# Kernel tuning notes

Hardware: AMD Instinct MI355X
Metric: run time of the kernel (lower is better)

Reference implementation:

```python
import jax, jax.numpy as jnp
import numpy as np

N_NODES = 50000
N_EDGES = 1600000
IN_DIM = 128
HIDDEN = 256
N_CLASSES = 2
N_GRAPHS = 512
BN_EPS = 1e-5


def setup_inputs() -> dict:
    key = jax.random.key(0)
    ks = jax.random.split(key, 12)
    x = jax.random.normal(ks[0], (N_NODES, IN_DIM), dtype=jnp.float32)
    edge_index = jax.random.randint(ks[1], (2, N_EDGES), 0, N_NODES, dtype=jnp.int64)
    batch = jnp.sort(jax.random.randint(ks[2], (N_NODES,), 0, N_GRAPHS, dtype=jnp.int64))
    s1 = 1.0 / np.sqrt(IN_DIM)
    s2 = 1.0 / np.sqrt(HIDDEN)
    return {
        "x": x,
        "edge_index": edge_index,
        "batch": batch,
        # GIN MLP: Linear(in,hidden) -> BN -> ReLU -> Linear(hidden,hidden)
        "W1": jax.random.uniform(ks[3], (IN_DIM, HIDDEN), jnp.float32, -s1, s1),
        "b1": jnp.zeros((HIDDEN,), jnp.float32),
        "g1": jnp.ones((HIDDEN,), jnp.float32),
        "be1": jnp.zeros((HIDDEN,), jnp.float32),
        "W2": jax.random.uniform(ks[4], (HIDDEN, HIDDEN), jnp.float32, -s2, s2),
        "b2": jnp.zeros((HIDDEN,), jnp.float32),
        # attention gate: Linear(hidden, 1)
        "Wg": jax.random.uniform(ks[5], (HIDDEN, 1), jnp.float32, -s2, s2),
        "bg": jnp.zeros((1,), jnp.float32),
        # head: BN(hidden) -> Dropout(eval: identity) -> Linear(hidden, n_classes)
        "g2": jnp.ones((HIDDEN,), jnp.float32),
        "be2": jnp.zeros((HIDDEN,), jnp.float32),
        "Wh": jax.random.uniform(ks[6], (HIDDEN, N_CLASSES), jnp.float32, -s2, s2),
        "bh": jnp.zeros((N_CLASSES,), jnp.float32),
    }


def _batchnorm(h, gamma, beta):
    # training-mode BN: batch statistics over axis 0 (biased variance, as torch)
    mu = jnp.mean(h, axis=0)
    var = jnp.mean(jnp.square(h - mu), axis=0)
    return gamma * (h - mu) * jax.lax.rsqrt(var + BN_EPS) + beta


def reference(x, edge_index, batch, W1, b1, g1, be1, W2, b2, Wg, bg, g2, be2, Wh, bh):
    src, dst = edge_index[0], edge_index[1]
    # GINConv (eps=0): agg_i = sum_{j->i} x_j ; h = MLP(x + agg)
    agg = jax.ops.segment_sum(x[src], dst, num_segments=N_NODES)  # [N, in_dim]
    h = x + agg
    h = h @ W1 + b1                      # [N, hidden]
    h = jax.nn.relu(_batchnorm(h, g1, be1))
    h = h @ W2 + b2                      # [N, hidden]
    h = jax.nn.relu(h)                   # outer F.relu in forward
    # AttentionalAggregation: segment softmax of gate, weighted sum per graph
    gate = h @ Wg + bg                   # [N, 1]
    m = jax.ops.segment_max(gate, batch, num_segments=N_GRAPHS)  # [G, 1]
    e = jnp.exp(gate - m[batch])
    s = jax.ops.segment_sum(e, batch, num_segments=N_GRAPHS)     # [G, 1]
    alpha = e / s[batch]                 # [N, 1]
    pooled = jax.ops.segment_sum(alpha * h, batch, num_segments=N_GRAPHS)  # [G, hidden]
    # head: BN -> (Dropout eval = identity) -> Linear -> log_softmax
    z = _batchnorm(pooled, g2, be2) @ Wh + bh  # [G, n_classes]
    return jax.nn.log_softmax(z, axis=-1)
```

## Files before the change

### kernel.cpp

```cpp
#include <hip/hip_runtime.h>

typedef unsigned int u32;
typedef unsigned short ushort_t;
typedef __attribute__((ext_vector_type(8))) short bf16x8;
typedef __attribute__((ext_vector_type(4))) float f32x4;

__device__ __forceinline__ float bf2f_lo(u32 u){
  union{u32 i; float f;} v; v.i = u<<16; return v.f;
}
__device__ __forceinline__ float bf2f_hi(u32 u){
  union{u32 i; float f;} v; v.i = u & 0xFFFF0000u; return v.f;
}
__device__ __forceinline__ float bf2f_s(ushort_t u){
  union{u32 i; float f;} v; v.i = ((u32)u)<<16; return v.f;
}
__device__ __forceinline__ u32 pack2bf(float a, float b){
  union{float f; u32 i;} va, vb; va.f=a; vb.f=b;
  u32 ra = (va.i + 0x7FFF + ((va.i>>16)&1)) >> 16;
  u32 rb = (vb.i + 0x7FFF + ((vb.i>>16)&1)) & 0xFFFF0000u;
  return ra | rb;
}
__device__ __forceinline__ ushort_t f2bf1(float f){
  union{float f; u32 i;} v; v.f=f;
  u32 r = v.i + 0x7FFF + ((v.i>>16)&1);
  return (ushort_t)(r>>16);
}

__global__ __launch_bounds__(256) void to_bf16(const float* __restrict__ x, u32* __restrict__ xb, long n4){
  long i = (long)blockIdx.x*256 + threadIdx.x;
  if(i*4 >= n4*4) return;
  float4 v = ((const float4*)x)[i];
  uint2 o; o.x = pack2bf(v.x, v.y); o.y = pack2bf(v.z, v.w);
  ((uint2*)xb)[i] = o;
}

__global__ __launch_bounds__(256) void transpose_w(const float* __restrict__ W, ushort_t* __restrict__ Wt, int K){
  int n = blockIdx.x;
  for(int k = threadIdx.x; k < K; k += 256){
    Wt[(size_t)n*K + k] = f2bf1(W[(size_t)k*256 + n]);
  }
}

__global__ __launch_bounds__(256) void hist_k(const int* __restrict__ dst, int* __restrict__ bcount,
                                              int E, int N, int NB){
  __shared__ int h[1024];
  for(int i=threadIdx.x; i<1024; i+=256) h[i]=0;
  __syncthreads();
  int e0 = blockIdx.x*8192;
  int e1 = min(e0+8192, E);
  for(int i=e0+threadIdx.x; i<e1; i+=256){
    int d = dst[i];
    if((u32)d >= (u32)N) d = 0;
    atomicAdd(&h[d>>6], 1);
  }
  __syncthreads();
  for(int i=threadIdx.x; i<NB; i+=256){
    int v = h[i];
    if(v) atomicAdd(&bcount[i], v);
  }
}

__global__ __launch_bounds__(256) void bucket_scan(const int* __restrict__ bcount, int* __restrict__ bstart,
                                                   int* __restrict__ bcursor, int NB){
  __shared__ int tsum[256];
  int t = threadIdx.x;
  int base = t*4;
  int a0 = (base+0<NB)?bcount[base+0]:0;
  int a1 = (base+1<NB)?bcount[base+1]:0;
  int a2 = (base+2<NB)?bcount[base+2]:0;
  int a3 = (base+3<NB)?bcount[base+3]:0;
  int s0=a0, s1=s0+a1, s2=s1+a2, s3=s2+a3;
  tsum[t]=s3; __syncthreads();
  #pragma unroll
  for(int d=1; d<256; d<<=1){
    int v = (t>=d)?tsum[t-d]:0;
    __syncthreads();
    tsum[t]+=v;
    __syncthreads();
  }
  int prev = (t>0)?tsum[t-1]:0;
  if(base+0<NB){ bstart[base+0]=prev;    bcursor[(base+0)*16]=0; }
  if(base+1<NB){ bstart[base+1]=prev+s0; bcursor[(base+1)*16]=0; }
  if(base+2<NB){ bstart[base+2]=prev+s1; bcursor[(base+2)*16]=0; }
  if(base+3<NB){ bstart[base+3]=prev+s2; bcursor[(base+3)*16]=0; }
  if(t==255){ bstart[NB]=prev+s3; }
}

__global__ __launch_bounds__(256) void binscatter2(const int* __restrict__ src, const int* __restrict__ dst,
                                                   const int* __restrict__ bstart, int* __restrict__ bcursor,
                                                   u32* __restrict__ pairs, int E, int N, int NB){
  __shared__ int hist[1024];
  __shared__ int base[1024];
  int e0 = blockIdx.x*8192;
  int e1 = min(e0+8192, E);
  for(int i=threadIdx.x; i<NB; i+=256) hist[i]=0;
  __syncthreads();
  for(int i=e0+threadIdx.x; i<e1; i+=256){
    int d = dst[i];
    if((u32)d >= (u32)N) d = 0;
    atomicAdd(&hist[d>>6], 1);
  }
  __syncthreads();
  for(int i=threadIdx.x; i<NB; i+=256){
    int c = hist[i];
    base[i] = c ? (bstart[i] + atomicAdd(&bcursor[i*16], c)) : 0;
    hist[i] = 0;
  }
  __syncthreads();
  for(int i=e0+threadIdx.x; i<e1; i+=256){
    int d = dst[i]; if((u32)d >= (u32)N) d = 0;
    int s = src[i]; if((u32)s >= (u32)N) s = 0;
    int b = d>>6;
    int loc = atomicAdd(&hist[b], 1);
    pairs[base[b]+loc] = (u32)s | (((u32)(d & 63))<<17);
  }
}

#define BCAP2 2560
__global__ __launch_bounds__(512) void gather_bucket(const u32* __restrict__ xb,
                                                     const u32* __restrict__ pairs,
                                                     const int* __restrict__ bstart,
                                                     u32* __restrict__ h0b, int N){
  __shared__ int lsrc[BCAP2];
  __shared__ int dcnt[32];
  __shared__ int dstart[33];
  __shared__ int dcur[32];
  __shared__ int s_fits;
  int b    = blockIdx.x >> 1;
  int half = blockIdx.x & 1;
  int p0 = bstart[b], p1 = bstart[b+1];
  int cnt = p1 - p0;
  int tid = threadIdx.x;
  if(tid < 32) dcnt[tid] = 0;
  __syncthreads();
  for(int i=tid; i<cnt; i+=512){
    u32 u = pairs[p0+i];
    int loc = (u>>17)&63;
    if((loc>>5) == half) atomicAdd(&dcnt[loc&31], 1);
  }
  __syncthreads();
  if(tid==0){
    int run=0;
    #pragma unroll
    for(int j=0;j<32;j++){ dstart[j]=run; dcur[j]=run; run+=dcnt[j]; }
    dstart[32]=run;
    s_fits = (run <= BCAP2) ? 1 : 0;
  }
  __syncthreads();
  bool fits = (s_fits != 0);
  if(fits){
    for(int i=tid; i<cnt; i+=512){
      u32 u = pairs[p0+i];
      int loc = (u>>17)&63;
      if((loc>>5) == half){
        int pos = atomicAdd(&dcur[loc&31], 1);
        lsrc[pos] = (int)(u & 0x1FFFFu);
      }
    }
    __syncthreads();
  }
  const uint4* xr = (const uint4*)xb;
  int slot = tid >> 4;
  int c = tid & 15;
  int node = b*64 + half*32 + slot;
  if(node >= N) return;
  uint4 xv = xr[(size_t)node*16 + c];
  float acc[8] = {
    bf2f_lo(xv.x), bf2f_hi(xv.x), bf2f_lo(xv.y), bf2f_hi(xv.y),
    bf2f_lo(xv.z), bf2f_hi(xv.z), bf2f_lo(xv.w), bf2f_hi(xv.w) };
  if(fits){
    int ds = dstart[slot], de = dstart[slot+1];
    int j = ds;
    for(; j+8 <= de; j += 8){
      int s0=lsrc[j+0], s1=lsrc[j+1], s2=lsrc[j+2], s3=lsrc[j+3];
      int s4=lsrc[j+4], s5=lsrc[j+5], s6=lsrc[j+6], s7=lsrc[j+7];
      uint4 v0 = xr[(size_t)s0*16 + c];
      uint4 v1 = xr[(size_t)s1*16 + c];
      uint4 v2 = xr[(size_t)s2*16 + c];
      uint4 v3 = xr[(size_t)s3*16 + c];
      uint4 v4 = xr[(size_t)s4*16 + c];
      uint4 v5 = xr[(size_t)s5*16 + c];
      uint4 v6 = xr[(size_t)s6*16 + c];
      uint4 v7 = xr[(size_t)s7*16 + c];
      acc[0]+=bf2f_lo(v0.x)+bf2f_lo(v1.x)+bf2f_lo(v2.x)+bf2f_lo(v3.x)
             +bf2f_lo(v4.x)+bf2f_lo(v5.x)+bf2f_lo(v6.x)+bf2f_lo(v7.x);
      acc[1]+=bf2f_hi(v0.x)+bf2f_hi(v1.x)+bf2f_hi(v2.x)+bf2f_hi(v3.x)
             +bf2f_hi(v4.x)+bf2f_hi(v5.x)+bf2f_hi(v6.x)+bf2f_hi(v7.x);
      acc[2]+=bf2f_lo(v0.y)+bf2f_lo(v1.y)+bf2f_lo(v2.y)+bf2f_lo(v3.y)
             +bf2f_lo(v4.y)+bf2f_lo(v5.y)+bf2f_lo(v6.y)+bf2f_lo(v7.y);
      acc[3]+=bf2f_hi(v0.y)+bf2f_hi(v1.y)+bf2f_hi(v2.y)+bf2f_hi(v3.y)
             +bf2f_hi(v4.y)+bf2f_hi(v5.y)+bf2f_hi(v6.y)+bf2f_hi(v7.y);
      acc[4]+=bf2f_lo(v0.z)+bf2f_lo(v1.z)+bf2f_lo(v2.z)+bf2f_lo(v3.z)
             +bf2f_lo(v4.z)+bf2f_lo(v5.z)+bf2f_lo(v6.z)+bf2f_lo(v7.z);
      acc[5]+=bf2f_hi(v0.z)+bf2f_hi(v1.z)+bf2f_hi(v2.z)+bf2f_hi(v3.z)
             +bf2f_hi(v4.z)+bf2f_hi(v5.z)+bf2f_hi(v6.z)+bf2f_hi(v7.z);
      acc[6]+=bf2f_lo(v0.w)+bf2f_lo(v1.w)+bf2f_lo(v2.w)+bf2f_lo(v3.w)
             +bf2f_lo(v4.w)+bf2f_lo(v5.w)+bf2f_lo(v6.w)+bf2f_lo(v7.w);
      acc[7]+=bf2f_hi(v0.w)+bf2f_hi(v1.w)+bf2f_hi(v2.w)+bf2f_hi(v3.w)
             +bf2f_hi(v4.w)+bf2f_hi(v5.w)+bf2f_hi(v6.w)+bf2f_hi(v7.w);
    }
    for(; j < de; j++){
      int s = lsrc[j];
      uint4 v = xr[(size_t)s*16 + c];
      acc[0]+=bf2f_lo(v.x); acc[1]+=bf2f_hi(v.x);
      acc[2]+=bf2f_lo(v.y); acc[3]+=bf2f_hi(v.y);
      acc[4]+=bf2f_lo(v.z); acc[5]+=bf2f_hi(v.z);
      acc[6]+=bf2f_lo(v.w); acc[7]+=bf2f_hi(v.w);
    }
  } else {
    int want = half*32 + slot;
    for(int i=0;i<cnt;i++){
      u32 u = pairs[p0+i];
      if((int)((u>>17)&63) == want){
        int s = (int)(u & 0x1FFFFu);
        uint4 v = xr[(size_t)s*16 + c];
        acc[0]+=bf2f_lo(v.x); acc[1]+=bf2f_hi(v.x);
        acc[2]+=bf2f_lo(v.y); acc[3]+=bf2f_hi(v.y);
        acc[4]+=bf2f_lo(v.z); acc[5]+=bf2f_hi(v.z);
        acc[6]+=bf2f_lo(v.w); acc[7]+=bf2f_hi(v.w);
      }
    }
  }
  uint4 o;
  o.x = pack2bf(acc[0],acc[1]); o.y = pack2bf(acc[2],acc[3]);
  o.z = pack2bf(acc[4],acc[5]); o.w = pack2bf(acc[6],acc[7]);
  ((uint4*)h0b)[(size_t)node*16 + c] = o;
}

template<int K, bool BNA, bool RELUOUT, bool GATE, bool ABF16, bool OUTBF16, bool STATS>
__global__ __launch_bounds__(512) void gemm_mfma(const void* __restrict__ Ap, const ushort_t* __restrict__ Wt,
                                                 const float* __restrict__ bias,
                                                 const float* __restrict__ scale, const float* __restrict__ shift,
                                                 void* __restrict__ Cp, int M,
                                                 const float* __restrict__ Wg, const float* __restrict__ bg,
                                                 float* __restrict__ gate,
                                                 float* __restrict__ psum, float* __restrict__ pq, int NS){
  __shared__ uint4 Al[8*129];
  __shared__ uint4 Bl[8*257];
  __shared__ float gacc[128];
  __shared__ float sstat[512];
  const int tid  = threadIdx.x;
  const int lane = tid & 63;
  const int wave = tid >> 6;
  const int lm   = lane & 15;
  const int q    = lane >> 4;
  const int mhalf= wave >> 2;
  const int nq   = wave & 3;
  const int m0   = blockIdx.x * 128;

  if(GATE && tid < 128) gacc[tid] = 0.f;
  if(STATS){ sstat[tid] = 0.f; }

  f32x4 acc[4][4];
  #pragma unroll
  for(int i=0;i<4;i++)
    #pragma unroll
    for(int j=0;j<4;j++) acc[i][j] = (f32x4){0.f,0.f,0.f,0.f};

  for(int k0=0; k0<K; k0+=64){
    #pragma unroll
    for(int i=0;i<2;i++){
      int idx = tid*2 + i;
      int m = idx >> 3, c = idx & 7;
      int grow = m0 + m;
      int kk = k0 + c*8;
      uint4 v = make_uint4(0,0,0,0);
      if(ABF16){
        if(grow < M) v = *(const uint4*)((const ushort_t*)Ap + (size_t)grow*K + kk);
        if(BNA){
          float f0=bf2f_lo(v.x), f1=bf2f_hi(v.x), f2=bf2f_lo(v.y), f3=bf2f_hi(v.y);
          float f4=bf2f_lo(v.z), f5=bf2f_hi(v.z), f6=bf2f_lo(v.w), f7=bf2f_hi(v.w);
          float4 s0 = *(const float4*)(scale+kk),  s1 = *(const float4*)(scale+kk+4);
          float4 t0 = *(const float4*)(shift+kk),  t1 = *(const float4*)(shift+kk+4);
          f0=fmaxf(fmaf(s0.x,f0,t0.x),0.f); f1=fmaxf(fmaf(s0.y,f1,t0.y),0.f);
          f2=fmaxf(fmaf(s0.z,f2,t0.z),0.f); f3=fmaxf(fmaf(s0.w,f3,t0.w),0.f);
          f4=fmaxf(fmaf(s1.x,f4,t1.x),0.f); f5=fmaxf(fmaf(s1.y,f5,t1.y),0.f);
          f6=fmaxf(fmaf(s1.z,f6,t1.z),0.f); f7=fmaxf(fmaf(s1.w,f7,t1.w),0.f);
          v.x = pack2bf(f0,f1); v.y = pack2bf(f2,f3);
          v.z = pack2bf(f4,f5); v.w = pack2bf(f6,f7);
        }
      } else {
        float4 u0 = make_float4(0,0,0,0), u1 = make_float4(0,0,0,0);
        if(grow < M){
          u0 = *(const float4*)((const float*)Ap + (size_t)grow*K + kk);
          u1 = *(const float4*)((const float*)Ap + (size_t)grow*K + kk + 4);
        }
        if(BNA){
          float4 s0 = *(const float4*)(scale+kk),  s1 = *(const float4*)(scale+kk+4);
          float4 t0 = *(const float4*)(shift+kk),  t1 = *(const float4*)(shift+kk+4);
          u0.x=fmaxf(fmaf(s0.x,u0.x,t0.x),0.f); u0.y=fmaxf(fmaf(s0.y,u0.y,t0.y),0.f);
          u0.z=fmaxf(fmaf(s0.z,u0.z,t0.z),0.f); u0.w=fmaxf(fmaf(s0.w,u0.w,t0.w),0.f);
          u1.x=fmaxf(fmaf(s1.x,u1.x,t1.x),0.f); u1.y=fmaxf(fmaf(s1.y,u1.y,t1.y),0.f);
          u1.z=fmaxf(fmaf(s1.z,u1.z,t1.z),0.f); u1.w=fmaxf(fmaf(s1.w,u1.w,t1.w),0.f);
        }
        v.x = pack2bf(u0.x,u0.y); v.y = pack2bf(u0.z,u0.w);
        v.z = pack2bf(u1.x,u1.y); v.w = pack2bf(u1.z,u1.w);
      }
      Al[c*129 + m] = v;
    }
    #pragma unroll
    for(int i=0;i<4;i++){
      int idx = tid*4 + i;
      int n = idx >> 3, c = idx & 7;
      Bl[c*257 + n] = *(const uint4*)(Wt + (size_t)n*K + k0 + c*8);
    }
    __syncthreads();
    #pragma unroll
    for(int ks=0; ks<2; ks++){
      int cc = ks*4 + q;
      bf16x8 af[4], bfr[4];
      #pragma unroll
      for(int mi=0; mi<4; mi++)
        af[mi] = *((const bf16x8*)&Al[cc*129 + mhalf*64 + mi*16 + lm]);
      #pragma unroll
      for(int ni=0; ni<4; ni++)
        bfr[ni] = *((const bf16x8*)&Bl[cc*257 + nq*64 + ni*16 + lm]);
      #pragma unroll
      for(int mi=0; mi<4; mi++)
        #pragma unroll
        for(int ni=0; ni<4; ni++)
          acc[mi][ni] = __builtin_amdgcn_mfma_f32_16x16x32_bf16(af[mi], bfr[ni], acc[mi][ni], 0, 0, 0);
    }
    __syncthreads();
  }

  float bb[4], wgv[4];
  float cs[4] = {0.f,0.f,0.f,0.f};
  float cq[4] = {0.f,0.f,0.f,0.f};
  #pragma unroll
  for(int ni=0; ni<4; ni++){
    int col = nq*64 + ni*16 + lm;
    bb[ni] = bias[col];
    if(GATE) wgv[ni] = Wg[col];
  }
  #pragma unroll
  for(int mi=0; mi<4; mi++){
    int rowloc0 = mhalf*64 + mi*16 + q*4;
    float gp[4] = {0.f,0.f,0.f,0.f};
    #pragma unroll
    for(int ni=0; ni<4; ni++){
      int col = nq*64 + ni*16 + lm;
      f32x4 o = acc[mi][ni];
      #pragma unroll
      for(int r=0; r<4; r++){
        float v = o[r] + bb[ni];
        if(RELUOUT) v = fmaxf(v, 0.f);
        int row = m0 + rowloc0 + r;
        if(row < M){
          if(OUTBF16) ((ushort_t*)Cp)[(size_t)row*256 + col] = f2bf1(v);
          else        ((float*)Cp)[(size_t)row*256 + col] = v;
          if(STATS){ cs[ni] += v; cq[ni] = fmaf(v, v, cq[ni]); }
        }
        if(GATE) gp[r] = fmaf(v, wgv[ni], gp[r]);
      }
    }
    if(GATE){
      #pragma unroll
      for(int r=0; r<4; r++){
        if(m0 + rowloc0 + r < M) atomicAdd(&gacc[rowloc0 + r], gp[r]);
      }
    }
  }
  if(STATS){
    __syncthreads();
    #pragma unroll
    for(int ni=0; ni<4; ni++){
      int col = nq*64 + ni*16 + lm;
      atomicAdd(&sstat[col], cs[ni]);
      atomicAdd(&sstat[256+col], cq[ni]);
    }
    __syncthreads();
    if(tid < 256){
      psum[(size_t)tid*NS + blockIdx.x] = sstat[tid];
      pq[(size_t)tid*NS + blockIdx.x]   = sstat[256+tid];
    }
  }
  if(GATE){
    __syncthreads();
    if(tid < 128){
      int row = m0 + tid;
      if(row < M) gate[row] = gacc[tid] + bg[0];
    }
  }
}

__global__ __launch_bounds__(256) void col_stats2(const float* __restrict__ h, float* __restrict__ psum,
                                                  float* __restrict__ pq, int M, int rpb, int nblk){
  int b = blockIdx.x;
  int g = threadIdx.x >> 6;
  int lane = threadIdx.x & 63;
  int c0 = lane*4;
  int r0 = b*rpb;
  int r1 = min(r0+rpb, M);
  float4 s4 = make_float4(0.f,0.f,0.f,0.f);
  float4 q4 = make_float4(0.f,0.f,0.f,0.f);
  for(int r=r0+g; r<r1; r+=4){
    float4 v = *(const float4*)(h + (size_t)r*256 + c0);
    s4.x+=v.x; s4.y+=v.y; s4.z+=v.z; s4.w+=v.w;
    q4.x=fmaf(v.x,v.x,q4.x); q4.y=fmaf(v.y,v.y,q4.y);
    q4.z=fmaf(v.z,v.z,q4.z); q4.w=fmaf(v.w,v.w,q4.w);
  }
  __shared__ float ls[1024];
  __shared__ float lq[1024];
  *(float4*)&ls[g*256+c0] = s4;
  *(float4*)&lq[g*256+c0] = q4;
  __syncthreads();
  if(threadIdx.x < 64){
    #pragma unroll
    for(int j=0;j<4;j++){
      int c = c0+j;
      float s = ls[c]+ls[256+c]+ls[512+c]+ls[768+c];
      float q = lq[c]+lq[256+c]+lq[512+c]+lq[768+c];
      psum[(size_t)c*nblk + b] = s;
      pq[(size_t)c*nblk + b]   = q;
    }
  }
}

__global__ __launch_bounds__(512) void stats_fin(const float* __restrict__ psum, const float* __restrict__ pq,
                                                 const float* __restrict__ gamma, const float* __restrict__ beta,
                                                 float* __restrict__ scale, float* __restrict__ shift,
                                                 int nblk, float invM){
  __shared__ float red[512];
  int t = threadIdx.x;
  const float* src = (t<256) ? (psum + (size_t)t*nblk) : (pq + (size_t)(t-256)*nblk);
  float s = 0.f;
  for(int i=0;i<nblk;i+=4){
    float4 v = *(const float4*)(src+i);
    s += v.x+v.y+v.z+v.w;
  }
  red[t]=s; __syncthreads();
  if(t<256){
    float mu  = red[t]*invM;
    float var = fmaxf(red[256+t]*invM - mu*mu, 0.f);
    float sc  = gamma[t] * rsqrtf(var + 1e-5f);
    scale[t]=sc; shift[t]=fmaf(-mu, sc, beta[t]);
  }
}

__global__ __launch_bounds__(512) void pool_k(const ushort_t* __restrict__ h2b, const float* __restrict__ gate,
                                              const int* __restrict__ batch, float* __restrict__ pooled, int N){
  int g = blockIdx.x;
  __shared__ int sb[2];
  __shared__ float red[8];
  __shared__ float s_m, s_inv;
  __shared__ float la[256];
  __shared__ float sa0[512];
  __shared__ float sa1[512];
  int t = threadIdx.x;
  if(t < 2){
    int target = g + t;
    int lo=0, hi=N;
    while(lo<hi){ int mid=(lo+hi)>>1; if(batch[mid] < target) lo=mid+1; else hi=mid; }
    sb[t] = lo;
  }
  __syncthreads();
  int beg = sb[0], end = sb[1];
  float mx = -1e30f;
  for(int i=beg+t; i<end; i+=512) mx = fmaxf(mx, gate[i]);
  #pragma unroll
  for(int d=32; d>0; d>>=1) mx = fmaxf(mx, __shfl_down(mx, d, 64));
  if((t&63)==0) red[t>>6] = mx;
  __syncthreads();
  if(t==0){
    float m = red[0];
    #pragma unroll
    for(int w=1; w<8; w++) m = fmaxf(m, red[w]);
    s_m = m;
  }
  __syncthreads();
  float m = s_m;
  float s = 0.f;
  for(int i=beg+t; i<end; i+=512) s += expf(gate[i]-m);
  #pragma unroll
  for(int d=32; d>0; d>>=1) s += __shfl_down(s, d, 64);
  if((t&63)==0) red[t>>6] = s;
  __syncthreads();
  if(t==0){
    float tot = 0.f;
    #pragma unroll
    for(int w=0; w<8; w++) tot += red[w];
    s_inv = (tot > 0.f) ? 1.f/tot : 0.f;
  }
  __syncthreads();
  float inv = s_inv;
  const u32* h2w = (const u32*)h2b;
  int colpair = t & 127;
  int rowgrp  = t >> 7;
  float a0 = 0.f, a1 = 0.f;
  for(int ci=beg; ci<end; ci+=256){
    int chunk = min(256, end-ci);
    if(t < 256) la[t] = (t < chunk) ? expf(gate[ci+t]-m)*inv : 0.f;
    __syncthreads();
    for(int j=rowgrp; j<chunk; j+=4){
      u32 h = h2w[(size_t)(ci+j)*128 + colpair];
      float w = la[j];
      a0 = fmaf(w, bf2f_lo(h), a0);
      a1 = fmaf(w, bf2f_hi(h), a1);
    }
    __syncthreads();
  }
  sa0[t] = a0; sa1[t] = a1;
  __syncthreads();
  if(t < 128){
    float r0 = sa0[t] + sa0[128+t] + sa0[256+t] + sa0[384+t];
    float r1 = sa1[t] + sa1[128+t] + sa1[256+t] + sa1[384+t];
    pooled[g*256 + t*2]   = r0;
    pooled[g*256 + t*2+1] = r1;
  }
}

__global__ __launch_bounds__(256) void head_k(const float* __restrict__ pooled,
                                              const float* __restrict__ sc2, const float* __restrict__ sh2,
                                              const float* __restrict__ Wh, const float* __restrict__ bh,
                                              float* __restrict__ out, int G){
  int w = (blockIdx.x*256 + threadIdx.x) >> 6;
  int l = threadIdx.x & 63;
  if(w >= G) return;
  float4 v  = *(const float4*)(pooled + (size_t)w*256 + l*4);
  float4 sc = *(const float4*)(sc2 + l*4);
  float4 sh = *(const float4*)(sh2 + l*4);
  float vv[4] = { fmaf(sc.x,v.x,sh.x), fmaf(sc.y,v.y,sh.y), fmaf(sc.z,v.z,sh.z), fmaf(sc.w,v.w,sh.w) };
  float4 w0 = *(const float4*)(Wh + (size_t)l*8);
  float4 w1 = *(const float4*)(Wh + (size_t)l*8 + 4);
  float a0 = vv[0]*w0.x + vv[1]*w0.z + vv[2]*w1.x + vv[3]*w1.z;
  float a1 = vv[0]*w0.y + vv[1]*w0.w + vv[2]*w1.y + vv[3]*w1.w;
  #pragma unroll
  for(int d=32; d>0; d>>=1){ a0 += __shfl_down(a0,d,64); a1 += __shfl_down(a1,d,64); }
  if(l==0){
    float z0 = a0 + bh[0];
    float z1 = a1 + bh[1];
    float mz = fmaxf(z0,z1);
    float lse = mz + logf(expf(z0-mz) + expf(z1-mz));
    out[w*2]   = z0 - lse;
    out[w*2+1] = z1 - lse;
  }
}

extern "C" void kernel_launch(void* const* d_in, const int* in_sizes, int n_in,
                              void* d_out, int out_size, void* d_ws, size_t ws_size,
                              hipStream_t stream){
  const float* x   = (const float*)d_in[0];
  const int*   ei  = (const int*)d_in[1];
  const int*   bat = (const int*)d_in[2];
  const float* W1  = (const float*)d_in[3];
  const float* b1  = (const float*)d_in[4];
  const float* g1  = (const float*)d_in[5];
  const float* be1 = (const float*)d_in[6];
  const float* W2  = (const float*)d_in[7];
  const float* b2  = (const float*)d_in[8];
  const float* Wg  = (const float*)d_in[9];
  const float* bg  = (const float*)d_in[10];
  const float* g2  = (const float*)d_in[11];
  const float* be2 = (const float*)d_in[12];
  const float* Wh  = (const float*)d_in[13];
  const float* bh  = (const float*)d_in[14];

  const int N = in_sizes[0] / 128;
  const int E = in_sizes[1] / 2;
  const int G = out_size / 2;
  const int NB = (N + 63) >> 6;
  const int NS1 = 512;
  const int NBLK2 = 64;

  char* ws = (char*)d_ws;
  u32*   h0b    = (u32*)ws;
  u32*   xb     = (u32*)(ws + 12800000);
  u32*   pairs  = (u32*)(ws + 25600000);
  int*   bcount = (int*)(ws + 32000000);
  int*   bstart = (int*)(ws + 32004352);
  int*   bcursor= (int*)(ws + 32008704);
  ushort_t* h2b = (ushort_t*)ws;
  u32*   h1b    = (u32*)(ws + 51200000);
  char*  p2 = ws + 102400000;
  float* psum1 = (float*)p2;          p2 += 256*NS1*4;
  float* pq1   = (float*)p2;          p2 += 256*NS1*4;
  float* psum2 = (float*)p2;          p2 += 256*NBLK2*4;
  float* pq2   = (float*)p2;          p2 += 256*NBLK2*4;
  float* sc1   = (float*)p2;          p2 += 1024;
  float* sh1   = (float*)p2;          p2 += 1024;
  float* gate  = (float*)p2;          p2 += (size_t)N*4 + 4096;
  float* pooled= (float*)p2;          p2 += (size_t)G*256*4;
  float* sc2   = (float*)p2;          p2 += 1024;
  float* sh2   = (float*)p2;          p2 += 1024;
  ushort_t* W1t = (ushort_t*)p2;      p2 += 256*128*2;
  ushort_t* W2t = (ushort_t*)p2;      p2 += 256*256*2;

  const int* src = ei;
  const int* dst = ei + E;

  hipMemsetAsync(bcount, 0, (size_t)NB*4, stream);
  hipMemsetAsync(psum1, 0, (size_t)256*NS1*4, stream);
  hipMemsetAsync(pq1,   0, (size_t)256*NS1*4, stream);

  transpose_w<<<256, 256, 0, stream>>>(W1, W1t, 128);
  transpose_w<<<256, 256, 0, stream>>>(W2, W2t, 256);
  long n4 = (long)N*128/4;
  to_bf16    <<<(int)((n4+255)/256), 256, 0, stream>>>(x, xb, n4);

  int nchunk = (E + 8191)/8192;
  hist_k     <<<nchunk, 256, 0, stream>>>(dst, bcount, E, N, NB);
  bucket_scan<<<1, 256, 0, stream>>>(bcount, bstart, bcursor, NB);
  binscatter2<<<nchunk, 256, 0, stream>>>(src, dst, bstart, bcursor, pairs, E, N, NB);
  gather_bucket<<<NB*2, 512, 0, stream>>>(xb, pairs, bstart, h0b, N);

  int gblocks = (N + 127)/128;
  gemm_mfma<128,false,false,false,true,true,true><<<gblocks, 512, 0, stream>>>(
      h0b, W1t, b1, nullptr, nullptr, h1b, N, nullptr, nullptr, nullptr, psum1, pq1, NS1);
  stats_fin  <<<1, 512, 0, stream>>>(psum1, pq1, g1, be1, sc1, sh1, NS1, 1.0f/(float)N);
  gemm_mfma<256,true,true,true,true,true,false><<<gblocks, 512, 0, stream>>>(
      h1b, W2t, b2, sc1, sh1, h2b, N, Wg, bg, gate, nullptr, nullptr, 0);

  pool_k <<<G, 512, 0, stream>>>(h2b, gate, bat, pooled, N);
  int rpb2 = (G + NBLK2 - 1)/NBLK2;
  col_stats2 <<<NBLK2, 256, 0, stream>>>(pooled, psum2, pq2, G, rpb2, NBLK2);
  stats_fin  <<<1, 512, 0, stream>>>(psum2, pq2, g2, be2, sc2, sh2, NBLK2, 1.0f/(float)G);
  head_k <<<(G+3)/4, 256, 0, stream>>>(pooled, sc2, sh2, Wh, bh, (float*)d_out, G);
}
```

Before: 353.8 us.

## Fuse prep kernels, drop bucket histogram/scan via fixed-capacity buckets, fuse head

Merges the bf16 conversion, both weight transposes and the cursor reset into one prep launch. Removes the histogram and scan passes by giving each 64-node bucket a fixed capacity, with an overflow list for edges past it. The gather now uses one block per bucket instead of two, and the head BN statistics, normalization and classifier run in a single one-block kernel. This cuts launches, memsets and a pass over dst, at the cost of a serial scan of the overflow list per node if any bucket overflows, and a single-block head.

```diff
diff --git a/kernel.cpp b/kernel.cpp
--- a/kernel.cpp
+++ b/kernel.cpp
@@ -4,6 +4,9 @@
 typedef unsigned short ushort_t;
 typedef __attribute__((ext_vector_type(8))) short bf16x8;
 typedef __attribute__((ext_vector_type(4))) float f32x4;
+
+#define PCAP 3072
+#define OVFCAP 1600000
 
 __device__ __forceinline__ float bf2f_lo(u32 u){
   union{u32 i; float f;} v; v.i = u<<16; return v.f;
@@ -26,69 +29,33 @@
   return (ushort_t)(r>>16);
 }
 
-__global__ __launch_bounds__(256) void to_bf16(const float* __restrict__ x, u32* __restrict__ xb, long n4){
-  long i = (long)blockIdx.x*256 + threadIdx.x;
-  if(i*4 >= n4*4) return;
-  float4 v = ((const float4*)x)[i];
-  uint2 o; o.x = pack2bf(v.x, v.y); o.y = pack2bf(v.z, v.w);
-  ((uint2*)xb)[i] = o;
-}
-
-__global__ __launch_bounds__(256) void transpose_w(const float* __restrict__ W, ushort_t* __restrict__ Wt, int K){
-  int n = blockIdx.x;
-  for(int k = threadIdx.x; k < K; k += 256){
-    Wt[(size_t)n*K + k] = f2bf1(W[(size_t)k*256 + n]);
-  }
-}
-
-__global__ __launch_bounds__(256) void hist_k(const int* __restrict__ dst, int* __restrict__ bcount,
-                                              int E, int N, int NB){
-  __shared__ int h[1024];
-  for(int i=threadIdx.x; i<1024; i+=256) h[i]=0;
-  __syncthreads();
-  int e0 = blockIdx.x*8192;
-  int e1 = min(e0+8192, E);
-  for(int i=e0+threadIdx.x; i<e1; i+=256){
-    int d = dst[i];
-    if((u32)d >= (u32)N) d = 0;
-    atomicAdd(&h[d>>6], 1);
-  }
-  __syncthreads();
-  for(int i=threadIdx.x; i<NB; i+=256){
-    int v = h[i];
-    if(v) atomicAdd(&bcount[i], v);
-  }
-}
-
-__global__ __launch_bounds__(256) void bucket_scan(const int* __restrict__ bcount, int* __restrict__ bstart,
-                                                   int* __restrict__ bcursor, int NB){
-  __shared__ int tsum[256];
-  int t = threadIdx.x;
-  int base = t*4;
-  int a0 = (base+0<NB)?bcount[base+0]:0;
-  int a1 = (base+1<NB)?bcount[base+1]:0;
-  int a2 = (base+2<NB)?bcount[base+2]:0;
-  int a3 = (base+3<NB)?bcount[base+3]:0;
-  int s0=a0, s1=s0+a1, s2=s1+a2, s3=s2+a3;
-  tsum[t]=s3; __syncthreads();
-  #pragma unroll
-  for(int d=1; d<256; d<<=1){
-    int v = (t>=d)?tsum[t-d]:0;
-    __syncthreads();
-    tsum[t]+=v;
-    __syncthreads();
-  }
-  int prev = (t>0)?tsum[t-1]:0;
-  if(base+0<NB){ bstart[base+0]=prev;    bcursor[(base+0)*16]=0; }
-  if(base+1<NB){ bstart[base+1]=prev+s0; bcursor[(base+1)*16]=0; }
-  if(base+2<NB){ bstart[base+2]=prev+s1; bcursor[(base+2)*16]=0; }
-  if(base+3<NB){ bstart[base+3]=prev+s2; bcursor[(base+3)*16]=0; }
-  if(t==255){ bstart[NB]=prev+s3; }
-}
-
-__global__ __launch_bounds__(256) void binscatter2(const int* __restrict__ src, const int* __restrict__ dst,
-                                                   const int* __restrict__ bstart, int* __restrict__ bcursor,
-                                                   u32* __restrict__ pairs, int E, int N, int NB){
+__global__ __launch_bounds__(256) void prep(const float* __restrict__ x, u32* __restrict__ xb, long nconv,
+                                            const float* __restrict__ W1, ushort_t* __restrict__ W1t,
+                                            const float* __restrict__ W2, ushort_t* __restrict__ W2t,
+                                            int* __restrict__ bcursor, int* __restrict__ ovf_cnt, int NB){
+  long blk = blockIdx.x;
+  int tid = threadIdx.x;
+  if(blk < nconv){
+    long i = blk*256 + tid;
+    float4 v = ((const float4*)x)[i];
+    uint2 o; o.x = pack2bf(v.x, v.y); o.y = pack2bf(v.z, v.w);
+    ((uint2*)xb)[i] = o;
+  } else if(blk < nconv + 256){
+    int n = (int)(blk - nconv);
+    for(int k = tid; k < 128; k += 256) W1t[(size_t)n*128 + k] = f2bf1(W1[(size_t)k*256 + n]);
+  } else if(blk < nconv + 512){
+    int n = (int)(blk - nconv - 256);
+    for(int k = tid; k < 256; k += 256) W2t[(size_t)n*256 + k] = f2bf1(W2[(size_t)k*256 + n]);
+  } else {
+    for(int i = tid; i < NB*16; i += 256) bcursor[i] = 0;
+    if(tid == 0) *ovf_cnt = 0;
+  }
+}
+
+__global__ __launch_bounds__(256) void binscatter_direct(const int* __restrict__ src, const int* __restrict__ dst,
+                                                         int* __restrict__ bcursor, u32* __restrict__ pairs,
+                                                         int* __restrict__ ovf, int* __restrict__ ovf_cnt,
+                                                         int E, int N, int NB){
   __shared__ int hist[1024];
   __shared__ int base[1024];
   int e0 = blockIdx.x*8192;
@@ -103,7 +70,7 @@
   __syncthreads();
   for(int i=threadIdx.x; i<NB; i+=256){
     int c = hist[i];
-    base[i] = c ? (bstart[i] + atomicAdd(&bcursor[i*16], c)) : 0;
+    base[i] = c ? atomicAdd(&bcursor[i*16], c) : 0;
     hist[i] = 0;
   }
   __syncthreads();
@@ -112,64 +79,66 @@
     int s = src[i]; if((u32)s >= (u32)N) s = 0;
     int b = d>>6;
     int loc = atomicAdd(&hist[b], 1);
-    pairs[base[b]+loc] = (u32)s | (((u32)(d & 63))<<17);
-  }
-}
-
-#define BCAP2 2560
+    int pos = base[b] + loc;
+    if(pos < PCAP){
+      pairs[(size_t)b*PCAP + pos] = (u32)s | (((u32)(d & 63))<<17);
+    } else {
+      int o = atomicAdd(ovf_cnt, 1);
+      if(o < OVFCAP){ ovf[2*o] = s; ovf[2*o+1] = d; }
+    }
+  }
+}
+
 __global__ __launch_bounds__(512) void gather_bucket(const u32* __restrict__ xb,
                                                      const u32* __restrict__ pairs,
-                                                     const int* __restrict__ bstart,
+                                                     const int* __restrict__ bcursor,
+                                                     const int* __restrict__ ovf, const int* __restrict__ ovf_cnt,
                                                      u32* __restrict__ h0b, int N){
-  __shared__ int lsrc[BCAP2];
-  __shared__ int dcnt[32];
-  __shared__ int dstart[33];
-  __shared__ int dcur[32];
-  __shared__ int s_fits;
-  int b    = blockIdx.x >> 1;
-  int half = blockIdx.x & 1;
-  int p0 = bstart[b], p1 = bstart[b+1];
-  int cnt = p1 - p0;
+  __shared__ int lsrc[PCAP];
+  __shared__ int dcnt[64];
+  __shared__ int dstart[65];
+  __shared__ int dcur[64];
+  __shared__ int s_ovfn;
+  int b = blockIdx.x;
   int tid = threadIdx.x;
-  if(tid < 32) dcnt[tid] = 0;
-  __syncthreads();
-  for(int i=tid; i<cnt; i+=512){
-    u32 u = pairs[p0+i];
-    int loc = (u>>17)&63;
-    if((loc>>5) == half) atomicAdd(&dcnt[loc&31], 1);
+  int cnt = bcursor[b*16];
+  if(cnt < 0) cnt = 0;
+  int cl = min(cnt, PCAP);
+  if(tid < 64) dcnt[tid] = 0;
+  if(tid == 0){ int o = *ovf_cnt; s_ovfn = (o < 0) ? 0 : min(o, OVFCAP); }
+  __syncthreads();
+  const u32* mypairs = pairs + (size_t)b*PCAP;
+  for(int i=tid; i<cl; i+=512){
+    u32 u = mypairs[i];
+    atomicAdd(&dcnt[(u>>17)&63], 1);
   }
   __syncthreads();
   if(tid==0){
     int run=0;
     #pragma unroll
-    for(int j=0;j<32;j++){ dstart[j]=run; dcur[j]=run; run+=dcnt[j]; }
-    dstart[32]=run;
-    s_fits = (run <= BCAP2) ? 1 : 0;
-  }
-  __syncthreads();
-  bool fits = (s_fits != 0);
-  if(fits){
-    for(int i=tid; i<cnt; i+=512){
-      u32 u = pairs[p0+i];
-      int loc = (u>>17)&63;
-      if((loc>>5) == half){
-        int pos = atomicAdd(&dcur[loc&31], 1);
-        lsrc[pos] = (int)(u & 0x1FFFFu);
-      }
-    }
-    __syncthreads();
-  }
+    for(int j=0;j<64;j++){ dstart[j]=run; dcur[j]=run; run+=dcnt[j]; }
+    dstart[64]=run;
+  }
+  __syncthreads();
+  for(int i=tid; i<cl; i+=512){
+    u32 u = mypairs[i];
+    int pos = atomicAdd(&dcur[(u>>17)&63], 1);
+    lsrc[pos] = (int)(u & 0x1FFFFu);
+  }
+  __syncthreads();
+  int ovfn = s_ovfn;
   const uint4* xr = (const uint4*)xb;
   int slot = tid >> 4;
   int c = tid & 15;
-  int node = b*64 + half*32 + slot;
-  if(node >= N) return;
-  uint4 xv = xr[(size_t)node*16 + c];
-  float acc[8] = {
-    bf2f_lo(xv.x), bf2f_hi(xv.x), bf2f_lo(xv.y), bf2f_hi(xv.y),
-    bf2f_lo(xv.z), bf2f_hi(xv.z), bf2f_lo(xv.w), bf2f_hi(xv.w) };
-  if(fits){
-    int ds = dstart[slot], de = dstart[slot+1];
+  for(int pass=0; pass<2; pass++){
+    int r = pass*32 + slot;
+    int node = b*64 + r;
+    if(node >= N) continue;
+    uint4 xv = xr[(size_t)node*16 + c];
+    float acc[8] = {
+      bf2f_lo(xv.x), bf2f_hi(xv.x), bf2f_lo(xv.y), bf2f_hi(xv.y),
+      bf2f_lo(xv.z), bf2f_hi(xv.z), bf2f_lo(xv.w), bf2f_hi(xv.w) };
+    int ds = dstart[r], de = dstart[r+1];
     int j = ds;
     for(; j+8 <= de; j += 8){
       int s0=lsrc[j+0], s1=lsrc[j+1], s2=lsrc[j+2], s3=lsrc[j+3];
@@ -207,24 +176,24 @@
       acc[4]+=bf2f_lo(v.z); acc[5]+=bf2f_hi(v.z);
       acc[6]+=bf2f_lo(v.w); acc[7]+=bf2f_hi(v.w);
     }
-  } else {
-    int want = half*32 + slot;
-    for(int i=0;i<cnt;i++){
-      u32 u = pairs[p0+i];
-      if((int)((u>>17)&63) == want){
-        int s = (int)(u & 0x1FFFFu);
-        uint4 v = xr[(size_t)s*16 + c];
-        acc[0]+=bf2f_lo(v.x); acc[1]+=bf2f_hi(v.x);
-        acc[2]+=bf2f_lo(v.y); acc[3]+=bf2f_hi(v.y);
-        acc[4]+=bf2f_lo(v.z); acc[5]+=bf2f_hi(v.z);
-        acc[6]+=bf2f_lo(v.w); acc[7]+=bf2f_hi(v.w);
+    if(ovfn > 0){
+      for(int i=0;i<ovfn;i++){
+        int s = ovf[2*i], d = ovf[2*i+1];
+        if(d == node){
+          if((u32)s >= (u32)N) s = 0;
+          uint4 v = xr[(size_t)s*16 + c];
+          acc[0]+=bf2f_lo(v.x); acc[1]+=bf2f_hi(v.x);
+          acc[2]+=bf2f_lo(v.y); acc[3]+=bf2f_hi(v.y);
+          acc[4]+=bf2f_lo(v.z); acc[5]+=bf2f_hi(v.z);
+          acc[6]+=bf2f_lo(v.w); acc[7]+=bf2f_hi(v.w);
+        }
       }
     }
-  }
-  uint4 o;
-  o.x = pack2bf(acc[0],acc[1]); o.y = pack2bf(acc[2],acc[3]);
-  o.z = pack2bf(acc[4],acc[5]); o.w = pack2bf(acc[6],acc[7]);
-  ((uint4*)h0b)[(size_t)node*16 + c] = o;
+    uint4 o;
+    o.x = pack2bf(acc[0],acc[1]); o.y = pack2bf(acc[2],acc[3]);
+    o.z = pack2bf(acc[4],acc[5]); o.w = pack2bf(acc[6],acc[7]);
+    ((uint4*)h0b)[(size_t)node*16 + c] = o;
+  }
 }
 
 template<int K, bool BNA, bool RELUOUT, bool GATE, bool ABF16, bool OUTBF16, bool STATS>
@@ -384,51 +353,20 @@
   }
 }
 
-__global__ __launch_bounds__(256) void col_stats2(const float* __restrict__ h, float* __restrict__ psum,
-                                                  float* __restrict__ pq, int M, int rpb, int nblk){
-  int b = blockIdx.x;
-  int g = threadIdx.x >> 6;
-  int lane = threadIdx.x & 63;
-  int c0 = lane*4;
-  int r0 = b*rpb;
-  int r1 = min(r0+rpb, M);
-  float4 s4 = make_float4(0.f,0.f,0.f,0.f);
-  float4 q4 = make_float4(0.f,0.f,0.f,0.f);
-  for(int r=r0+g; r<r1; r+=4){
-    float4 v = *(const float4*)(h + (size_t)r*256 + c0);
-    s4.x+=v.x; s4.y+=v.y; s4.z+=v.z; s4.w+=v.w;
-    q4.x=fmaf(v.x,v.x,q4.x); q4.y=fmaf(v.y,v.y,q4.y);
-    q4.z=fmaf(v.z,v.z,q4.z); q4.w=fmaf(v.w,v.w,q4.w);
-  }
-  __shared__ float ls[1024];
-  __shared__ float lq[1024];
-  *(float4*)&ls[g*256+c0] = s4;
-  *(float4*)&lq[g*256+c0] = q4;
-  __syncthreads();
-  if(threadIdx.x < 64){
-    #pragma unroll
-    for(int j=0;j<4;j++){
-      int c = c0+j;
-      float s = ls[c]+ls[256+c]+ls[512+c]+ls[768+c];
-      float q = lq[c]+lq[256+c]+lq[512+c]+lq[768+c];
-      psum[(size_t)c*nblk + b] = s;
-      pq[(size_t)c*nblk + b]   = q;
-    }
-  }
-}
-
 __global__ __launch_bounds__(512) void stats_fin(const float* __restrict__ psum, const float* __restrict__ pq,
                                                  const float* __restrict__ gamma, const float* __restrict__ beta,
                                                  float* __restrict__ scale, float* __restrict__ shift,
-                                                 int nblk, float invM){
+                                                 int nblk, int NS, float invM){
   __shared__ float red[512];
   int t = threadIdx.x;
-  const float* src = (t<256) ? (psum + (size_t)t*nblk) : (pq + (size_t)(t-256)*nblk);
+  const float* src = (t<256) ? (psum + (size_t)t*NS) : (pq + (size_t)(t-256)*NS);
   float s = 0.f;
-  for(int i=0;i<nblk;i+=4){
+  int i = 0;
+  for(; i+4 <= nblk; i += 4){
     float4 v = *(const float4*)(src+i);
     s += v.x+v.y+v.z+v.w;
   }
+  for(; i < nblk; i++) s += src[i];
   red[t]=s; __syncthreads();
   if(t<256){
     float mu  = red[t]*invM;
@@ -510,30 +448,48 @@
   }
 }
 
-__global__ __launch_bounds__(256) void head_k(const float* __restrict__ pooled,
-                                              const float* __restrict__ sc2, const float* __restrict__ sh2,
-                                              const float* __restrict__ Wh, const float* __restrict__ bh,
-                                              float* __restrict__ out, int G){
-  int w = (blockIdx.x*256 + threadIdx.x) >> 6;
-  int l = threadIdx.x & 63;
-  if(w >= G) return;
-  float4 v  = *(const float4*)(pooled + (size_t)w*256 + l*4);
-  float4 sc = *(const float4*)(sc2 + l*4);
-  float4 sh = *(const float4*)(sh2 + l*4);
-  float vv[4] = { fmaf(sc.x,v.x,sh.x), fmaf(sc.y,v.y,sh.y), fmaf(sc.z,v.z,sh.z), fmaf(sc.w,v.w,sh.w) };
-  float4 w0 = *(const float4*)(Wh + (size_t)l*8);
-  float4 w1 = *(const float4*)(Wh + (size_t)l*8 + 4);
-  float a0 = vv[0]*w0.x + vv[1]*w0.z + vv[2]*w1.x + vv[3]*w1.z;
-  float a1 = vv[0]*w0.y + vv[1]*w0.w + vv[2]*w1.y + vv[3]*w1.w;
-  #pragma unroll
-  for(int d=32; d>0; d>>=1){ a0 += __shfl_down(a0,d,64); a1 += __shfl_down(a1,d,64); }
-  if(l==0){
+__global__ __launch_bounds__(512) void head_fused(const float* __restrict__ pooled,
+                                                  const float* __restrict__ g2, const float* __restrict__ be2,
+                                                  const float* __restrict__ Wh, const float* __restrict__ bh,
+                                                  float* __restrict__ out, int G){
+  __shared__ float red[512];
+  __shared__ float sc[256], sh[256];
+  __shared__ float wh[512];
+  int t = threadIdx.x;
+  {
+    int c = t & 255;
+    bool wantq = (t >= 256);
+    float s = 0.f;
+    for(int r=0; r<G; r++){
+      float v = pooled[(size_t)r*256 + c];
+      s = wantq ? fmaf(v, v, s) : (s + v);
+    }
+    red[t] = s;
+  }
+  if(t < 512) wh[t] = Wh[t];
+  __syncthreads();
+  if(t < 256){
+    float invG = 1.f/(float)G;
+    float mu  = red[t]*invG;
+    float var = fmaxf(red[256+t]*invG - mu*mu, 0.f);
+    float s   = g2[t] * rsqrtf(var + 1e-5f);
+    sc[t] = s; sh[t] = fmaf(-mu, s, be2[t]);
+  }
+  __syncthreads();
+  if(t < G){
+    float a0 = 0.f, a1 = 0.f;
+    const float* row = pooled + (size_t)t*256;
+    for(int c=0; c<256; c++){
+      float vv = fmaf(sc[c], row[c], sh[c]);
+      a0 = fmaf(vv, wh[2*c],   a0);
+      a1 = fmaf(vv, wh[2*c+1], a1);
+    }
     float z0 = a0 + bh[0];
     float z1 = a1 + bh[1];
     float mz = fmaxf(z0,z1);
     float lse = mz + logf(expf(z0-mz) + expf(z1-mz));
-    out[w*2]   = z0 - lse;
-    out[w*2+1] = z1 - lse;
+    out[t*2]   = z0 - lse;
+    out[t*2+1] = z1 - lse;
   }
 }
 
@@ -560,60 +516,44 @@
   const int E = in_sizes[1] / 2;
   const int G = out_size / 2;
   const int NB = (N + 63) >> 6;
-  const int NS1 = 512;
-  const int NBLK2 = 64;
+  const int gblocks = (N + 127)/128;
+  const int NS1 = (gblocks + 7) & ~7;
 
   char* ws = (char*)d_ws;
   u32*   h0b    = (u32*)ws;
   u32*   xb     = (u32*)(ws + 12800000);
   u32*   pairs  = (u32*)(ws + 25600000);
-  int*   bcount = (int*)(ws + 32000000);
-  int*   bstart = (int*)(ws + 32004352);
-  int*   bcursor= (int*)(ws + 32008704);
+  int*   bcursor= (int*)(ws + 35210240);
+  int*   ovf_cnt= (int*)(ws + 35275776);
+  int*   ovf    = (int*)(ws + 35276032);
   ushort_t* h2b = (ushort_t*)ws;
   u32*   h1b    = (u32*)(ws + 51200000);
   char*  p2 = ws + 102400000;
   float* psum1 = (float*)p2;          p2 += 256*NS1*4;
   float* pq1   = (float*)p2;          p2 += 256*NS1*4;
-  float* psum2 = (float*)p2;          p2 += 256*NBLK2*4;
-  float* pq2   = (float*)p2;          p2 += 256*NBLK2*4;
   float* sc1   = (float*)p2;          p2 += 1024;
   float* sh1   = (float*)p2;          p2 += 1024;
   float* gate  = (float*)p2;          p2 += (size_t)N*4 + 4096;
   float* pooled= (float*)p2;          p2 += (size_t)G*256*4;
-  float* sc2   = (float*)p2;          p2 += 1024;
-  float* sh2   = (float*)p2;          p2 += 1024;
   ushort_t* W1t = (ushort_t*)p2;      p2 += 256*128*2;
   ushort_t* W2t = (ushort_t*)p2;      p2 += 256*256*2;
 
   const int* src = ei;
   const int* dst = ei + E;
 
-  hipMemsetAsync(bcount, 0, (size_t)NB*4, stream);
-  hipMemsetAsync(psum1, 0, (size_t)256*NS1*4, stream);
-  hipMemsetAsync(pq1,   0, (size_t)256*NS1*4, stream);
-
-  transpose_w<<<256, 256, 0, stream>>>(W1, W1t, 128);
-  transpose_w<<<256, 256, 0, stream>>>(W2, W2t, 256);
-  long n4 = (long)N*128/4;
-  to_bf16    <<<(int)((n4+255)/256), 256, 0, stream>>>(x, xb, n4);
+  long nconv = (long)N*128/4/256;
+  prep<<<(int)(nconv + 512 + 1), 256, 0, stream>>>(x, xb, nconv, W1, W1t, W2, W2t, bcursor, ovf_cnt, NB);
 
   int nchunk = (E + 8191)/8192;
-  hist_k     <<<nchunk, 256, 0, stream>>>(dst, bcount, E, N, NB);
-  bucket_scan<<<1, 256, 0, stream>>>(bcount, bstart, bcursor, NB);
-  binscatter2<<<nchunk, 256, 0, stream>>>(src, dst, bstart, bcursor, pairs, E, N, NB);
-  gather_bucket<<<NB*2, 512, 0, stream>>>(xb, pairs, bstart, h0b, N);
-
-  int gblocks = (N + 127)/128;
+  binscatter_direct<<<nchunk, 256, 0, stream>>>(src, dst, bcursor, pairs, ovf, ovf_cnt, E, N, NB);
+  gather_bucket<<<NB, 512, 0, stream>>>(xb, pairs, bcursor, ovf, ovf_cnt, h0b, N);
+
   gemm_mfma<128,false,false,false,true,true,true><<<gblocks, 512, 0, stream>>>(
       h0b, W1t, b1, nullptr, nullptr, h1b, N, nullptr, nullptr, nullptr, psum1, pq1, NS1);
-  stats_fin  <<<1, 512, 0, stream>>>(psum1, pq1, g1, be1, sc1, sh1, NS1, 1.0f/(float)N);
+  stats_fin<<<1, 512, 0, stream>>>(psum1, pq1, g1, be1, sc1, sh1, gblocks, NS1, 1.0f/(float)N);
   gemm_mfma<256,true,true,true,true,true,false><<<gblocks, 512, 0, stream>>>(
       h1b, W2t, b2, sc1, sh1, h2b, N, Wg, bg, gate, nullptr, nullptr, 0);
 
-  pool_k <<<G, 512, 0, stream>>>(h2b, gate, bat, pooled, N);
-  int rpb2 = (G + NBLK2 - 1)/NBLK2;
-  col_stats2 <<<NBLK2, 256, 0, stream>>>(pooled, psum2, pq2, G, rpb2, NBLK2);
-  stats_fin  <<<1, 512, 0, stream>>>(psum2, pq2, g2, be2, sc2, sh2, NBLK2, 1.0f/(float)G);
-  head_k <<<(G+3)/4, 256, 0, stream>>>(pooled, sc2, sh2, Wh, bh, (float*)d_out, G);
-}
+  pool_k<<<G, 512, 0, stream>>>(h2b, gate, bat, pooled, N);
+  head_fused<<<1, 512, 0, stream>>>(pooled, g2, be2, Wh, bh, (float*)d_out, G);
+}
```

Result: slower. 477.3 us (+34.9%).
